# Performance work log

Measured on AMD Instinct MI355X. Metric: run time of the kernel, lower is better.

## Reference

```python
import jax, jax.numpy as jnp
import numpy as np

B, S, D, H = 8, 1024, 1024, 16
HD = D // H  # head_size = 64


def layernorm(x, g, b, eps=1e-5):
    mu = jnp.mean(x, axis=-1, keepdims=True)
    var = jnp.var(x, axis=-1, keepdims=True)
    return (x - mu) * jax.lax.rsqrt(var + eps) * g + b


def setup_inputs() -> dict:
    key = jax.random.key(0)
    ks = jax.random.split(key, 12)
    s_attn = 1.0 / np.sqrt(D)
    inp = {
        "x": jax.random.normal(ks[0], (B, S, D), dtype=jnp.float32),
        # per-head q/k/v projections (bias=False), stacked: [H, D, HD]
        "Wq": jax.random.normal(ks[1], (H, D, HD), dtype=jnp.float32) * s_attn,
        "Wk": jax.random.normal(ks[2], (H, D, HD), dtype=jnp.float32) * s_attn,
        "Wv": jax.random.normal(ks[3], (H, D, HD), dtype=jnp.float32) * s_attn,
        "Wo": jax.random.normal(ks[4], (D, D), dtype=jnp.float32) * s_attn,
        "bo": jnp.zeros((D,), dtype=jnp.float32),
        # FFN: hidden = 1 * n_embd (as in source)
        "W1": jax.random.normal(ks[5], (D, D), dtype=jnp.float32) * s_attn,
        "b1": jnp.zeros((D,), dtype=jnp.float32),
        "W2": jax.random.normal(ks[6], (D, D), dtype=jnp.float32) * s_attn,
        "b2": jnp.zeros((D,), dtype=jnp.float32),
        "g_ln1": jnp.ones((D,), dtype=jnp.float32),
        "b_ln1": jnp.zeros((D,), dtype=jnp.float32),
        "g_ln2": jnp.ones((D,), dtype=jnp.float32),
        "b_ln2": jnp.zeros((D,), dtype=jnp.float32),
    }
    return inp


def reference(x, Wq, Wk, Wv, Wo, bo, W1, b1, W2, b2, g_ln1, b_ln1, g_ln2, b_ln2):
    # pre-LN self-attention
    h = layernorm(x, g_ln1, b_ln1)
    q = jnp.einsum("bsd,hde->bhse", h, Wq)
    k = jnp.einsum("bsd,hde->bhse", h, Wk)
    v = jnp.einsum("bsd,hde->bhse", h, Wv)
    scale = HD ** -0.5  # k.shape[-1] ** -0.5
    wei = jax.nn.softmax(jnp.einsum("bhse,bhte->bhst", q, k) * scale, axis=-1)
    attn = jnp.einsum("bhst,bhte->bhse", wei, v)  # [B,H,S,HD]
    # concat heads (head order matches torch.cat over head list)
    attn = attn.transpose(0, 2, 1, 3).reshape(B, S, D)
    sa = attn @ Wo + bo
    x = x + sa
    # pre-LN FFN with exact GELU (torch nn.GELU default)
    h2 = layernorm(x, g_ln2, b_ln2)
    ff = jax.nn.gelu(h2 @ W1 + b1, approximate=False) @ W2 + b2
    return x + ff
```

## Files before the change

### kernel.cpp

```cpp
#include <hip/hip_runtime.h>
#include <hip/hip_bf16.h>
#include <math.h>

#define B_ 8
#define S_ 1024
#define D_ 1024
#define H_ 16
#define HD_ 64

typedef __bf16 bf16x8 __attribute__((ext_vector_type(8)));
typedef __bf16 bf16x4 __attribute__((ext_vector_type(4)));
typedef float f32x4 __attribute__((ext_vector_type(4)));

#define FMAX3(a, b, c) fmaxf(fmaxf((a), (b)), (c))

__device__ __forceinline__ void gld_lds16(const __bf16* g, __bf16* l) {
  __builtin_amdgcn_global_load_lds(
      (const __attribute__((address_space(1))) void*)g,
      (__attribute__((address_space(3))) void*)l, 16, 0, 0);
}

__global__ __launch_bounds__(256) void ln_kernel(const float* __restrict__ x,
                                                 const float* __restrict__ g,
                                                 const float* __restrict__ b,
                                                 __bf16* __restrict__ out) {
  int row = blockIdx.x;
  const float* xr = x + (size_t)row * D_;
  __bf16* outr = out + (size_t)row * D_;
  int tid = threadIdx.x;

  float4 v = ((const float4*)xr)[tid];
  float s = v.x + v.y + v.z + v.w;
  float ss = v.x * v.x + v.y * v.y + v.z * v.z + v.w * v.w;

  #pragma unroll
  for (int m = 1; m < 64; m <<= 1) {
    s += __shfl_xor(s, m);
    ss += __shfl_xor(ss, m);
  }
  __shared__ float red[10];
  int wid = tid >> 6;
  if ((tid & 63) == 0) { red[wid] = s; red[4 + wid] = ss; }
  __syncthreads();
  if (tid == 0) {
    float ts = red[0] + red[1] + red[2] + red[3];
    float tss = red[4] + red[5] + red[6] + red[7];
    float mu = ts * (1.0f / D_);
    float var = tss * (1.0f / D_) - mu * mu;
    red[8] = mu;
    red[9] = rsqrtf(var + 1e-5f);
  }
  __syncthreads();
  float mu = red[8], rstd = red[9];
  float4 gv = ((const float4*)g)[tid];
  float4 bv = ((const float4*)b)[tid];
  bf16x4 o;
  o[0] = (__bf16)((v.x - mu) * rstd * gv.x + bv.x);
  o[1] = (__bf16)((v.y - mu) * rstd * gv.y + bv.y);
  o[2] = (__bf16)((v.z - mu) * rstd * gv.z + bv.z);
  o[3] = (__bf16)((v.w - mu) * rstd * gv.w + bv.w);
  *(bf16x4*)(outr + tid * 4) = o;
}

__global__ __launch_bounds__(256) void transpose_all(const float* __restrict__ Wq,
                                                     const float* __restrict__ Wk,
                                                     const float* __restrict__ Wv,
                                                     const float* __restrict__ Wo,
                                                     const float* __restrict__ W1,
                                                     const float* __restrict__ W2,
                                                     __bf16* __restrict__ out) {
  __shared__ float t[64][65];
  const int x = blockIdx.x, y = blockIdx.y, z = blockIdx.z;
  const int tid = threadIdx.x;
  const int r = tid >> 4, c4 = (tid & 15) * 4;

  const float* src;
  int stride, orowbase, kbase;
  if (z < 3) {
    const float* W = (z == 0 ? Wq : z == 1 ? Wk : Wv);
    src = W + (size_t)y * (D_ * HD_) + (size_t)(x * 64) * HD_;
    stride = HD_;
    orowbase = z * 1024 + y * 64;
    kbase = x * 64;
  } else {
    const float* W = (z == 3 ? Wo : z == 4 ? W1 : W2);
    src = W + (size_t)(y * 64) * D_ + x * 64;
    stride = D_;
    orowbase = z * 1024 + x * 64;
    kbase = y * 64;
  }

  #pragma unroll
  for (int i = 0; i < 4; ++i) {
    float4 v = *(const float4*)&src[(size_t)(i * 16 + r) * stride + c4];
    t[i * 16 + r][c4 + 0] = v.x;
    t[i * 16 + r][c4 + 1] = v.y;
    t[i * 16 + r][c4 + 2] = v.z;
    t[i * 16 + r][c4 + 3] = v.w;
  }
  __syncthreads();
  #pragma unroll
  for (int i = 0; i < 4; ++i) {
    bf16x4 o;
    #pragma unroll
    for (int j = 0; j < 4; ++j) o[j] = (__bf16)t[c4 + j][i * 16 + r];
    *(bf16x4*)&out[(size_t)(orowbase + i * 16 + r) * 1024 + kbase + c4] = o;
  }
}

#define MODE_QKV 0
#define MODE_PROJ 1
#define MODE_FF1 2
#define MODE_FF2 3

#define QSCALE 0.18033688011112042f

template <int MODE>
__global__ __launch_bounds__(256) void gemm_mfma(const __bf16* __restrict__ A,
                                                 const __bf16* __restrict__ Bt,
                                                 const float* __restrict__ bias,
                                                 const float* __restrict__ resid,
                                                 float* __restrict__ outf,
                                                 __bf16* __restrict__ outb,
                                                 int M, int N, int K) {
  __shared__ __align__(16) __bf16 As[128 * 64];
  __shared__ __align__(16) __bf16 Bs[128 * 64];
  const int tid = threadIdx.x;

  const int gx = (int)gridDim.x;
  const int nwg = gx * (int)gridDim.y;
  const int flat = (int)blockIdx.y * gx + (int)blockIdx.x;
  const int wg = (flat & 7) * (nwg >> 3) + (flat >> 3);
  const int m0 = (wg / gx) * 128, n0 = (wg % gx) * 128;

  const int w = tid >> 6, l = tid & 63, lr = l & 15, lg = l >> 4;
  const int wm = (w >> 1) * 64, wn = (w & 1) * 64;

  f32x4 acc[4][4] = {};

  for (int k0 = 0; k0 < K; k0 += 64) {
    __syncthreads();
    #pragma unroll
    for (int i = 0; i < 4; ++i) {
      int e = i * 256 + tid;
      int row = e >> 3;
      int col = ((e & 7) ^ (row & 7)) * 8;
      gld_lds16(A + (size_t)(m0 + row) * K + k0 + col, &As[e * 8]);
    }
    #pragma unroll
    for (int i = 0; i < 4; ++i) {
      int e = i * 256 + tid;
      int row = e >> 3;
      int col = ((e & 7) ^ (row & 7)) * 8;
      gld_lds16(Bt + (size_t)(n0 + row) * K + k0 + col, &Bs[e * 8]);
    }
    asm volatile("s_waitcnt vmcnt(0)");
    __syncthreads();

    #pragma unroll
    for (int kk = 0; kk < 2; ++kk) {
      bf16x8 af[4], bfr[4];
      #pragma unroll
      for (int i = 0; i < 4; ++i)
        af[i] = *(const bf16x8*)
            &As[((wm + i * 16 + lr) * 8 + ((kk * 4 + lg) ^ (lr & 7))) * 8];
      #pragma unroll
      for (int j = 0; j < 4; ++j)
        bfr[j] = *(const bf16x8*)
            &Bs[((wn + j * 16 + lr) * 8 + ((kk * 4 + lg) ^ (lr & 7))) * 8];
      #pragma unroll
      for (int i = 0; i < 4; ++i)
        #pragma unroll
        for (int j = 0; j < 4; ++j)
          acc[i][j] = __builtin_amdgcn_mfma_f32_16x16x32_bf16(af[i], bfr[j], acc[i][j], 0, 0, 0);
    }
  }

  #pragma unroll
  for (int i = 0; i < 4; ++i) {
    #pragma unroll
    for (int j = 0; j < 4; ++j) {
      #pragma unroll
      for (int r = 0; r < 4; ++r) {
        int m = m0 + wm + i * 16 + 4 * lg + r;
        int n = n0 + wn + j * 16 + lr;
        float val = acc[i][j][r];
        if (MODE == MODE_QKV) {
          int b = m >> 10, s = m & 1023;
          int which = n >> 10, hh = (n >> 6) & 15, e = n & 63;
          if (which == 0) val *= QSCALE;
          outb[(size_t)which * 8388608 + ((size_t)(b * 16 + hh) * 1024 + s) * 64 + e] =
              (__bf16)val;
        } else if (MODE == MODE_PROJ) {
          size_t idx = (size_t)m * 1024 + n;
          outf[idx] = resid[idx] + val + bias[n];
        } else if (MODE == MODE_FF1) {
          val += bias[n];
          outb[(size_t)m * 1024 + n] =
              (__bf16)(0.5f * val * (1.0f + erff(val * 0.70710678118654752f)));
        } else {
          size_t idx = (size_t)m * 1024 + n;
          outf[idx] = outf[idx] + val + bias[n];
        }
      }
    }
  }
}

__global__ __launch_bounds__(512) void fattn(const __bf16* __restrict__ q,
                                             const __bf16* __restrict__ k,
                                             const __bf16* __restrict__ v,
                                             __bf16* __restrict__ outC) {
  __shared__ __align__(16) __bf16 Klds[2][64 * 64];
  __shared__ __align__(16) __bf16 Vp[2][64 * 64];

  const int bid = blockIdx.x;
  const int bh = (bid & 7) * 16 + ((bid >> 3) & 15);
  const int qt = bid >> 7;
  const int tid = threadIdx.x;
  const int w = tid >> 6, l = tid & 63;
  const int lr = l & 15, lg = l >> 4;

  const size_t base = (size_t)bh * (S_ * HD_);
  const int qrow0 = qt * 128 + w * 16;
  const __bf16* kg = k + base;
  const __bf16* vg = v + base;

  const int krow = tid >> 3;
  const int kcol = ((tid & 7) ^ (krow & 7)) * 8;
  const int vc = (l & 0x20) + ((l & 0xC) << 1) + ((l & 0x10) >> 2) + (l & 3);
  const int vchi = vc >> 3, vclo = vc & 7;

  bf16x8 qf0, qf1;
  {
    const __bf16* qp = q + base + (size_t)(qrow0 + lr) * HD_ + lg * 8;
    qf0 = *(const bf16x8*)(qp);
    qf1 = *(const bf16x8*)(qp + 32);
  }

  const __bf16 onev = (lr == 0) ? (__bf16)1.0f : (__bf16)0.0f;
  const bf16x8 vones = {onev, onev, onev, onev, onev, onev, onev, onev};

  f32x4 oacc[5] = {};
  float m_run = -1e30f;

  gld_lds16(kg + (size_t)krow * HD_ + kcol, &Klds[0][tid * 8]);
  bf16x8 vr;
  {
    vr = *(const bf16x8*)(vg + (size_t)l * HD_ + w * 8);
    #pragma unroll
    for (int i = 0; i < 8; ++i)
      Vp[0][(w * 8 + i) * 64 + ((vchi ^ i) << 3) + vclo] = vr[i];
    vr = *(const bf16x8*)(vg + (size_t)(64 + l) * HD_ + w * 8);
  }
  asm volatile("s_waitcnt vmcnt(0)");
  __syncthreads();

  int cur = 0;
  for (int t = 0; t < 16; ++t) {
    {
      int tn = (t < 15) ? (t + 1) : 15;
      gld_lds16(kg + ((size_t)tn * 64 + krow) * HD_ + kcol, &Klds[cur ^ 1][tid * 8]);
    }

    f32x4 sacc[4];
    const __bf16* kb = &Klds[cur][0];
    __builtin_amdgcn_s_setprio(1);
    #pragma unroll
    for (int g = 0; g < 4; ++g) {
      bf16x8 kf0 = *(const bf16x8*)&kb[((16 * g + lr) * 8 + (lg ^ (lr & 7))) * 8];
      bf16x8 kf1 = *(const bf16x8*)&kb[((16 * g + lr) * 8 + ((lg + 4) ^ (lr & 7))) * 8];
      f32x4 z = {0.f, 0.f, 0.f, 0.f};
      z = __builtin_amdgcn_mfma_f32_16x16x32_bf16(kf0, qf0, z, 0, 0, 0);
      sacc[g] = __builtin_amdgcn_mfma_f32_16x16x32_bf16(kf1, qf1, z, 0, 0, 0);
    }
    __builtin_amdgcn_s_setprio(0);

    float m0 = FMAX3(sacc[0][0], sacc[0][1], sacc[0][2]);
    float m1 = FMAX3(sacc[0][3], sacc[1][0], sacc[1][1]);
    float m2 = FMAX3(sacc[1][2], sacc[1][3], sacc[2][0]);
    float m3 = FMAX3(sacc[2][1], sacc[2][2], sacc[2][3]);
    float m4 = FMAX3(sacc[3][0], sacc[3][1], sacc[3][2]);
    float tm = FMAX3(FMAX3(m0, m1, m2), FMAX3(m3, m4, sacc[3][3]), m_run);
    tm = fmaxf(tm, __shfl_xor(tm, 16));
    tm = fmaxf(tm, __shfl_xor(tm, 32));

    if (!__all(tm - m_run <= 11.5f)) {
      float corr = exp2f(m_run - tm);
      m_run = tm;
      #pragma unroll
      for (int r = 0; r < 4; ++r) {
        float cq = __shfl(corr, 4 * lg + r);
        #pragma unroll
        for (int g = 0; g < 5; ++g) oacc[g][r] *= cq;
      }
    }

    float p[4][4];
    #pragma unroll
    for (int g = 0; g < 4; ++g)
      #pragma unroll
      for (int r = 0; r < 4; ++r) p[g][r] = exp2f(sacc[g][r] - m_run);

    #pragma unroll
    for (int i = 0; i < 8; ++i)
      Vp[cur ^ 1][(w * 8 + i) * 64 + ((vchi ^ i) << 3) + vclo] = vr[i];
    {
      int tnn = (t < 14) ? (t + 2) : 15;
      vr = *(const bf16x8*)(vg + ((size_t)tnn * 64 + l) * HD_ + w * 8);
    }

    bf16x8 af0, af1;
    #pragma unroll
    for (int j = 0; j < 8; ++j) {
      af0[j] = (__bf16)p[j >> 2][j & 3];
      af1[j] = (__bf16)p[2 + (j >> 2)][j & 3];
    }
    __builtin_amdgcn_s_setprio(1);
    #pragma unroll
    for (int g = 0; g < 4; ++g) {
      bf16x8 vf0 = *(const bf16x8*)&Vp[cur][(16 * g + lr) * 64 + ((lg ^ (lr & 7)) << 3)];
      bf16x8 vf1 = *(const bf16x8*)&Vp[cur][(16 * g + lr) * 64 + (((lg + 4) ^ (lr & 7)) << 3)];
      oacc[g] = __builtin_amdgcn_mfma_f32_16x16x32_bf16(af0, vf0, oacc[g], 0, 0, 0);
      oacc[g] = __builtin_amdgcn_mfma_f32_16x16x32_bf16(af1, vf1, oacc[g], 0, 0, 0);
    }
    oacc[4] = __builtin_amdgcn_mfma_f32_16x16x32_bf16(af0, vones, oacc[4], 0, 0, 0);
    oacc[4] = __builtin_amdgcn_mfma_f32_16x16x32_bf16(af1, vones, oacc[4], 0, 0, 0);
    __builtin_amdgcn_s_setprio(0);

    asm volatile("s_waitcnt vmcnt(0)");
    __syncthreads();
    cur ^= 1;
  }

  const int b = bh >> 4, hh = bh & 15;
  #pragma unroll
  for (int r = 0; r < 4; ++r) {
    float linv = 1.0f / __shfl(oacc[4][r], l & 48);
    int srow = qrow0 + 4 * lg + r;
    __bf16* op = outC + ((size_t)(b * S_ + srow)) * D_ + hh * HD_;
    #pragma unroll
    for (int g = 0; g < 4; ++g) op[16 * g + lr] = (__bf16)(oacc[g][r] * linv);
  }
}

extern "C" void kernel_launch(void* const* d_in, const int* in_sizes, int n_in,
                              void* d_out, int out_size, void* d_ws, size_t ws_size,
                              hipStream_t stream) {
  const float* x   = (const float*)d_in[0];
  const float* Wq  = (const float*)d_in[1];
  const float* Wk  = (const float*)d_in[2];
  const float* Wv  = (const float*)d_in[3];
  const float* Wo  = (const float*)d_in[4];
  const float* bo  = (const float*)d_in[5];
  const float* W1  = (const float*)d_in[6];
  const float* b1  = (const float*)d_in[7];
  const float* W2  = (const float*)d_in[8];
  const float* b2  = (const float*)d_in[9];
  const float* g1  = (const float*)d_in[10];
  const float* bl1 = (const float*)d_in[11];
  const float* g2  = (const float*)d_in[12];
  const float* bl2 = (const float*)d_in[13];
  float* out = (float*)d_out;

  const size_t MN = (size_t)B_ * S_ * D_;
  __bf16* h     = (__bf16*)d_ws;
  __bf16* wt    = h + MN;
  __bf16* qkv   = wt + (size_t)6144 * 1024;
  __bf16* attnC = qkv + 3 * MN;
  __bf16* ff1   = attnC + MN;

  __bf16* wqkv_t = wt;
  __bf16* wo_t   = wt + (size_t)3072 * 1024;
  __bf16* w1_t   = wt + (size_t)4096 * 1024;
  __bf16* w2_t   = wt + (size_t)5120 * 1024;

  const int rows = B_ * S_;

  ln_kernel<<<rows, 256, 0, stream>>>(x, g1, bl1, h);
  transpose_all<<<dim3(16, 16, 6), 256, 0, stream>>>(Wq, Wk, Wv, Wo, W1, W2, wt);

  gemm_mfma<MODE_QKV><<<dim3(24, 64), 256, 0, stream>>>(
      h, wqkv_t, nullptr, nullptr, nullptr, qkv, rows, 3072, D_);
  fattn<<<1024, 512, 0, stream>>>(qkv, qkv + MN, qkv + 2 * MN, attnC);
  gemm_mfma<MODE_PROJ><<<dim3(8, 64), 256, 0, stream>>>(
      attnC, wo_t, bo, x, out, nullptr, rows, D_, D_);
  ln_kernel<<<rows, 256, 0, stream>>>(out, g2, bl2, h);
  gemm_mfma<MODE_FF1><<<dim3(8, 64), 256, 0, stream>>>(
      h, w1_t, b1, nullptr, nullptr, ff1, rows, D_, D_);
  gemm_mfma<MODE_FF2><<<dim3(8, 64), 256, 0, stream>>>(
      ff1, w2_t, b2, nullptr, out, nullptr, rows, D_, D_);
}
```

Baseline: 253.1 us.

## Store residual stream in bf16 and loosen attention loop waits

```diff
diff --git a/kernel.cpp b/kernel.cpp
--- a/kernel.cpp
+++ b/kernel.cpp
@@ -20,10 +20,10 @@
       (__attribute__((address_space(3))) void*)l, 16, 0, 0);
 }
 
-__global__ __launch_bounds__(256) void ln_kernel(const float* __restrict__ x,
-                                                 const float* __restrict__ g,
-                                                 const float* __restrict__ b,
-                                                 __bf16* __restrict__ out) {
+__global__ __launch_bounds__(256) void ln_f32(const float* __restrict__ x,
+                                              const float* __restrict__ g,
+                                              const float* __restrict__ b,
+                                              __bf16* __restrict__ out) {
   int row = blockIdx.x;
   const float* xr = x + (size_t)row * D_;
   __bf16* outr = out + (size_t)row * D_;
@@ -59,6 +59,49 @@
   o[1] = (__bf16)((v.y - mu) * rstd * gv.y + bv.y);
   o[2] = (__bf16)((v.z - mu) * rstd * gv.z + bv.z);
   o[3] = (__bf16)((v.w - mu) * rstd * gv.w + bv.w);
+  *(bf16x4*)(outr + tid * 4) = o;
+}
+
+__global__ __launch_bounds__(256) void ln_bf16(const __bf16* __restrict__ x,
+                                               const float* __restrict__ g,
+                                               const float* __restrict__ b,
+                                               __bf16* __restrict__ out) {
+  int row = blockIdx.x;
+  const __bf16* xr = x + (size_t)row * D_;
+  __bf16* outr = out + (size_t)row * D_;
+  int tid = threadIdx.x;
+
+  bf16x4 xv = *(const bf16x4*)(xr + tid * 4);
+  float v0 = (float)xv[0], v1 = (float)xv[1], v2 = (float)xv[2], v3 = (float)xv[3];
+  float s = v0 + v1 + v2 + v3;
+  float ss = v0 * v0 + v1 * v1 + v2 * v2 + v3 * v3;
+
+  #pragma unroll
+  for (int m = 1; m < 64; m <<= 1) {
+    s += __shfl_xor(s, m);
+    ss += __shfl_xor(ss, m);
+  }
+  __shared__ float red[10];
+  int wid = tid >> 6;
+  if ((tid & 63) == 0) { red[wid] = s; red[4 + wid] = ss; }
+  __syncthreads();
+  if (tid == 0) {
+    float ts = red[0] + red[1] + red[2] + red[3];
+    float tss = red[4] + red[5] + red[6] + red[7];
+    float mu = ts * (1.0f / D_);
+    float var = tss * (1.0f / D_) - mu * mu;
+    red[8] = mu;
+    red[9] = rsqrtf(var + 1e-5f);
+  }
+  __syncthreads();
+  float mu = red[8], rstd = red[9];
+  float4 gv = ((const float4*)g)[tid];
+  float4 bv = ((const float4*)b)[tid];
+  bf16x4 o;
+  o[0] = (__bf16)((v0 - mu) * rstd * gv.x + bv.x);
+  o[1] = (__bf16)((v1 - mu) * rstd * gv.y + bv.y);
+  o[2] = (__bf16)((v2 - mu) * rstd * gv.z + bv.z);
+  o[3] = (__bf16)((v3 - mu) * rstd * gv.w + bv.w);
   *(bf16x4*)(outr + tid * 4) = o;
 }
 
@@ -119,7 +162,8 @@
 __global__ __launch_bounds__(256) void gemm_mfma(const __bf16* __restrict__ A,
                                                  const __bf16* __restrict__ Bt,
                                                  const float* __restrict__ bias,
-                                                 const float* __restrict__ resid,
+                                                 const float* __restrict__ residf,
+                                                 const __bf16* __restrict__ residb,
                                                  float* __restrict__ outf,
                                                  __bf16* __restrict__ outb,
                                                  int M, int N, int K) {
@@ -193,14 +237,14 @@
               (__bf16)val;
         } else if (MODE == MODE_PROJ) {
           size_t idx = (size_t)m * 1024 + n;
-          outf[idx] = resid[idx] + val + bias[n];
+          outb[idx] = (__bf16)(residf[idx] + val + bias[n]);
         } else if (MODE == MODE_FF1) {
           val += bias[n];
           outb[(size_t)m * 1024 + n] =
               (__bf16)(0.5f * val * (1.0f + erff(val * 0.70710678118654752f)));
         } else {
           size_t idx = (size_t)m * 1024 + n;
-          outf[idx] = outf[idx] + val + bias[n];
+          outf[idx] = (float)residb[idx] + val + bias[n];
         }
       }
     }
@@ -253,8 +297,10 @@
       Vp[0][(w * 8 + i) * 64 + ((vchi ^ i) << 3) + vclo] = vr[i];
     vr = *(const bf16x8*)(vg + (size_t)(64 + l) * HD_ + w * 8);
   }
-  asm volatile("s_waitcnt vmcnt(0)");
-  __syncthreads();
+  asm volatile("s_waitcnt vmcnt(1) lgkmcnt(0)" ::: "memory");
+  __builtin_amdgcn_sched_barrier(0);
+  __builtin_amdgcn_s_barrier();
+  __builtin_amdgcn_sched_barrier(0);
 
   int cur = 0;
   for (int t = 0; t < 16; ++t) {
@@ -275,6 +321,14 @@
       sacc[g] = __builtin_amdgcn_mfma_f32_16x16x32_bf16(kf1, qf1, z, 0, 0, 0);
     }
     __builtin_amdgcn_s_setprio(0);
+
+    #pragma unroll
+    for (int i = 0; i < 8; ++i)
+      Vp[cur ^ 1][(w * 8 + i) * 64 + ((vchi ^ i) << 3) + vclo] = vr[i];
+    {
+      int tnn = (t < 14) ? (t + 2) : 15;
+      vr = *(const bf16x8*)(vg + ((size_t)tnn * 64 + l) * HD_ + w * 8);
+    }
 
     float m0 = FMAX3(sacc[0][0], sacc[0][1], sacc[0][2]);
     float m1 = FMAX3(sacc[0][3], sacc[1][0], sacc[1][1]);
@@ -286,7 +340,7 @@
     tm = fmaxf(tm, __shfl_xor(tm, 32));
 
     if (!__all(tm - m_run <= 11.5f)) {
-      float corr = exp2f(m_run - tm);
+      float corr = __builtin_amdgcn_exp2f(m_run - tm);
       m_run = tm;
       #pragma unroll
       for (int r = 0; r < 4; ++r) {
@@ -300,15 +354,8 @@
     #pragma unroll
     for (int g = 0; g < 4; ++g)
       #pragma unroll
-      for (int r = 0; r < 4; ++r) p[g][r] = exp2f(sacc[g][r] - m_run);
-
-    #pragma unroll
-    for (int i = 0; i < 8; ++i)
-      Vp[cur ^ 1][(w * 8 + i) * 64 + ((vchi ^ i) << 3) + vclo] = vr[i];
-    {
-      int tnn = (t < 14) ? (t + 2) : 15;
-      vr = *(const bf16x8*)(vg + ((size_t)tnn * 64 + l) * HD_ + w * 8);
-    }
+      for (int r = 0; r < 4; ++r)
+        p[g][r] = __builtin_amdgcn_exp2f(sacc[g][r] - m_run);
 
     bf16x8 af0, af1;
     #pragma unroll
@@ -328,8 +375,10 @@
     oacc[4] = __builtin_amdgcn_mfma_f32_16x16x32_bf16(af1, vones, oacc[4], 0, 0, 0);
     __builtin_amdgcn_s_setprio(0);
 
-    asm volatile("s_waitcnt vmcnt(0)");
-    __syncthreads();
+    asm volatile("s_waitcnt vmcnt(1) lgkmcnt(0)" ::: "memory");
+    __builtin_amdgcn_sched_barrier(0);
+    __builtin_amdgcn_s_barrier();
+    __builtin_amdgcn_sched_barrier(0);
     cur ^= 1;
   }
 
@@ -369,6 +418,7 @@
   __bf16* qkv   = wt + (size_t)6144 * 1024;
   __bf16* attnC = qkv + 3 * MN;
   __bf16* ff1   = attnC + MN;
+  __bf16* mid   = ff1 + MN;
 
   __bf16* wqkv_t = wt;
   __bf16* wo_t   = wt + (size_t)3072 * 1024;
@@ -377,17 +427,17 @@
 
   const int rows = B_ * S_;
 
-  ln_kernel<<<rows, 256, 0, stream>>>(x, g1, bl1, h);
+  ln_f32<<<rows, 256, 0, stream>>>(x, g1, bl1, h);
   transpose_all<<<dim3(16, 16, 6), 256, 0, stream>>>(Wq, Wk, Wv, Wo, W1, W2, wt);
 
   gemm_mfma<MODE_QKV><<<dim3(24, 64), 256, 0, stream>>>(
-      h, wqkv_t, nullptr, nullptr, nullptr, qkv, rows, 3072, D_);
+      h, wqkv_t, nullptr, nullptr, nullptr, nullptr, qkv, rows, 3072, D_);
   fattn<<<1024, 512, 0, stream>>>(qkv, qkv + MN, qkv + 2 * MN, attnC);
   gemm_mfma<MODE_PROJ><<<dim3(8, 64), 256, 0, stream>>>(
-      attnC, wo_t, bo, x, out, nullptr, rows, D_, D_);
-  ln_kernel<<<rows, 256, 0, stream>>>(out, g2, bl2, h);
+      attnC, wo_t, bo, x, nullptr, nullptr, mid, rows, D_, D_);
+  ln_bf16<<<rows, 256, 0, stream>>>(mid, g2, bl2, h);
   gemm_mfma<MODE_FF1><<<dim3(8, 64), 256, 0, stream>>>(
-      h, w1_t, b1, nullptr, nullptr, ff1, rows, D_, D_);
+      h, w1_t, b1, nullptr, nullptr, nullptr, ff1, rows, D_, D_);
   gemm_mfma<MODE_FF2><<<dim3(8, 64), 256, 0, stream>>>(
-      ff1, w2_t, b2, nullptr, out, nullptr, rows, D_, D_);
-}
+      ff1, w2_t, b2, nullptr, mid, out, nullptr, rows, D_, D_);
+}
```

After: 234.4 us. 1.08x faster.
